# Kernel optimization log

Measured on AMD Instinct MI355X. Metric: run time of the kernel, lower is better.

The kernel has to match this reference:

```python
import jax, jax.numpy as jnp
import numpy as np

H, W = 4096, 4096
KH, KW = 16, 16


def setup_inputs() -> dict:
    key = jax.random.key(0)
    kx, kw = jax.random.split(key)
    x = jax.random.normal(kx, (H, W), dtype=jnp.float32)
    weight = jax.random.normal(kw, (KH, KW), dtype=jnp.float32)
    bias = jnp.zeros((1,), dtype=jnp.float32)
    return {"x": x, "weight": weight, "bias": bias}


def reference(x, weight, bias):
    # 2D valid cross-correlation (no kernel flip), single channel, + scalar bias.
    # lax.conv_general_dilated computes cross-correlation by default.
    lhs = x[None, None, :, :]          # [1,1,H,W]
    rhs = weight[None, None, :, :]     # [1,1,KH,KW]
    y = jax.lax.conv_general_dilated(
        lhs, rhs,
        window_strides=(1, 1),
        padding="VALID",
        dimension_numbers=("NCHW", "OIHW", "NCHW"),
    )[0, 0]                            # [H-KH+1, W-KW+1]
    return y + bias[0]
```

## Files before the change

### kernel.cpp

```cpp
#include <hip/hip_runtime.h>

#define IH 4096
#define IW 4096
#define KH 16
#define KW 16
#define OH 4081
#define OW 4081

#define TBR 64
#define TBC 256
#define LROWS 79
#define LCH 40
#define LSTR (LCH*8)

typedef short bf16x8 __attribute__((ext_vector_type(8)));
typedef float f32x16 __attribute__((ext_vector_type(16)));

static __device__ __forceinline__ unsigned int f2bf(float f) {
    unsigned int u = __float_as_uint(f);
    return (u + 0x7FFFu + ((u >> 16) & 1u)) >> 16;
}

__global__ void build_B(const float* __restrict__ wgt, unsigned short* __restrict__ Bt) {
    int idx = blockIdx.x * 256 + threadIdx.x;
    if (idx >= 16 * 32 * 48) return;
    int vp = idx % 48;
    int n  = (idx / 48) & 31;
    int u  = idx / (48 * 32);
    int t  = vp - n;
    float val = (t >= 0 && t < KW) ? wgt[u * KW + t] : 0.0f;
    Bt[idx] = (unsigned short)f2bf(val);
}

__global__ __launch_bounds__(256, 3)
void conv_mfma32(const float* __restrict__ x,
                 const unsigned short* __restrict__ Bt,
                 const float* __restrict__ bias,
                 float* __restrict__ out) {
    __shared__ unsigned short tile[LROWS * LSTR];

    const int tid  = threadIdx.x;
    const int lane = tid & 63;
    const int wv   = tid >> 6;
    const int rb   = wv >> 1;
    const int cb   = wv & 1;
    const int m    = lane & 31;
    const int hi   = lane >> 5;
    const int gy0  = blockIdx.y * TBR;
    const int gx0  = blockIdx.x * TBC;

    for (int idx = tid; idx < LROWS * 34; idx += 256) {
        int row = idx / 34;
        int c   = idx - row * 34;
        int gy  = gy0 + row;
        int gx  = gx0 + 8 * c;
        float4 q0 = make_float4(0.f, 0.f, 0.f, 0.f);
        float4 q1 = q0;
        if (gy < IH && gx < IW) {
            q0 = *reinterpret_cast<const float4*>(x + (size_t)gy * IW + gx);
            q1 = *reinterpret_cast<const float4*>(x + (size_t)gy * IW + gx + 4);
        }
        uint4 p;
        p.x = f2bf(q0.x) | (f2bf(q0.y) << 16);
        p.y = f2bf(q0.z) | (f2bf(q0.w) << 16);
        p.z = f2bf(q1.x) | (f2bf(q1.y) << 16);
        p.w = f2bf(q1.z) | (f2bf(q1.w) << 16);
        int s    = (row ^ (row >> 3)) & 7;
        int phys = c ^ s;
        *reinterpret_cast<uint4*>(&tile[row * LSTR + phys * 8]) = p;
    }
    __syncthreads();

    f32x16 acc0 = {0,0,0,0,0,0,0,0,0,0,0,0,0,0,0,0};
    f32x16 acc1 = {0,0,0,0,0,0,0,0,0,0,0,0,0,0,0,0};
    f32x16 acc2 = {0,0,0,0,0,0,0,0,0,0,0,0,0,0,0,0};
    f32x16 acc3 = {0,0,0,0,0,0,0,0,0,0,0,0,0,0,0,0};

    const int cB = cb * 16 + hi;
    const unsigned short* Blane = Bt + m * 48 + hi * 8;

    bf16x8 bc0 = *reinterpret_cast<const bf16x8*>(Blane + 0);
    bf16x8 bc1 = *reinterpret_cast<const bf16x8*>(Blane + 16);
    bf16x8 bc2 = *reinterpret_cast<const bf16x8*>(Blane + 32);

#pragma unroll
    for (int u = 0; u < KH; ++u) {
        bf16x8 bn0 = bc0, bn1 = bc1, bn2 = bc2;
        if (u + 1 < KH) {
            const unsigned short* Bu = Blane + (u + 1) * (32 * 48);
            bn0 = *reinterpret_cast<const bf16x8*>(Bu + 0);
            bn1 = *reinterpret_cast<const bf16x8*>(Bu + 16);
            bn2 = *reinterpret_cast<const bf16x8*>(Bu + 32);
        }

        const int rowA = rb * 32 + m + u;
        const int s    = (rowA ^ (rowA >> 3)) & 7;
        const unsigned short* rbase = &tile[rowA * LSTR];

        bf16x8 a[9];
#pragma unroll
        for (int d = 0; d < 9; ++d) {
            int phys = (cB + 2 * d) ^ s;
            a[d] = *reinterpret_cast<const bf16x8*>(rbase + phys * 8);
        }

        acc0 = __builtin_amdgcn_mfma_f32_32x32x16_bf16(a[0], bc0, acc0, 0, 0, 0);
        acc0 = __builtin_amdgcn_mfma_f32_32x32x16_bf16(a[1], bc1, acc0, 0, 0, 0);
        acc0 = __builtin_amdgcn_mfma_f32_32x32x16_bf16(a[2], bc2, acc0, 0, 0, 0);
        acc1 = __builtin_amdgcn_mfma_f32_32x32x16_bf16(a[2], bc0, acc1, 0, 0, 0);
        acc1 = __builtin_amdgcn_mfma_f32_32x32x16_bf16(a[3], bc1, acc1, 0, 0, 0);
        acc1 = __builtin_amdgcn_mfma_f32_32x32x16_bf16(a[4], bc2, acc1, 0, 0, 0);
        acc2 = __builtin_amdgcn_mfma_f32_32x32x16_bf16(a[4], bc0, acc2, 0, 0, 0);
        acc2 = __builtin_amdgcn_mfma_f32_32x32x16_bf16(a[5], bc1, acc2, 0, 0, 0);
        acc2 = __builtin_amdgcn_mfma_f32_32x32x16_bf16(a[6], bc2, acc2, 0, 0, 0);
        acc3 = __builtin_amdgcn_mfma_f32_32x32x16_bf16(a[6], bc0, acc3, 0, 0, 0);
        acc3 = __builtin_amdgcn_mfma_f32_32x32x16_bf16(a[7], bc1, acc3, 0, 0, 0);
        acc3 = __builtin_amdgcn_mfma_f32_32x32x16_bf16(a[8], bc2, acc3, 0, 0, 0);

        bc0 = bn0; bc1 = bn1; bc2 = bn2;
    }

    const float bv   = bias[0];
    const int   row0 = gy0 + rb * 32 + 4 * hi;
    const int   col0 = gx0 + cb * 128 + m;
    const bool  full = (gy0 + TBR <= OH) && (gx0 + TBC <= OW);

    const f32x16* accs[4] = {&acc0, &acc1, &acc2, &acc3};
#pragma unroll
    for (int g = 0; g < 4; ++g) {
        const f32x16 acc = *accs[g];
        const int col = col0 + g * 32;
        float* op = out + col;
        if (full) {
#pragma unroll
            for (int r = 0; r < 16; ++r) {
                int rr = row0 + (r & 3) + 8 * (r >> 2);
                op[(size_t)rr * OW] = acc[r] + bv;
            }
        } else if (col < OW) {
#pragma unroll
            for (int r = 0; r < 16; ++r) {
                int rr = row0 + (r & 3) + 8 * (r >> 2);
                if (rr < OH) op[(size_t)rr * OW] = acc[r] + bv;
            }
        }
    }
}

extern "C" void kernel_launch(void* const* d_in, const int* in_sizes, int n_in,
                              void* d_out, int out_size, void* d_ws, size_t ws_size,
                              hipStream_t stream) {
    const float* x  = (const float*)d_in[0];
    const float* w  = (const float*)d_in[1];
    const float* b  = (const float*)d_in[2];
    float* out = (float*)d_out;
    unsigned short* Bt = (unsigned short*)d_ws;

    build_B<<<96, 256, 0, stream>>>(w, Bt);

    dim3 grid((OW + TBC - 1) / TBC, (OH + TBR - 1) / TBR);
    conv_mfma32<<<grid, dim3(256), 0, stream>>>(x, Bt, b, out);
}
```

Measured before the change: 137.7 us.

## Halve column tile width, drop LDS swizzle, raise occupancy target

Shrinks the block tile from 256 to 128 output columns, so each wave keeps two MFMA accumulators instead of four and the shared tile shrinks. The launch bound is raised so more blocks can be resident per CU. The XOR swizzle on the LDS tile is replaced by a padded row stride of 168 elements, which is meant to avoid bank conflicts more cheaply. In exchange, the halo columns (extra input read and converted per block) make up a larger share of each tile, and there is less reuse of A fragments per wave.

```diff
diff --git a/kernel.cpp b/kernel.cpp
--- a/kernel.cpp
+++ b/kernel.cpp
@@ -8,10 +8,9 @@
 #define OW 4081
 
 #define TBR 64
-#define TBC 256
+#define TBC 128
 #define LROWS 79
-#define LCH 40
-#define LSTR (LCH*8)
+#define LSTR 168
 
 typedef short bf16x8 __attribute__((ext_vector_type(8)));
 typedef float f32x16 __attribute__((ext_vector_type(16)));
@@ -32,7 +31,7 @@
     Bt[idx] = (unsigned short)f2bf(val);
 }
 
-__global__ __launch_bounds__(256, 3)
+__global__ __launch_bounds__(256, 6)
 void conv_mfma32(const float* __restrict__ x,
                  const unsigned short* __restrict__ Bt,
                  const float* __restrict__ bias,
@@ -49,9 +48,9 @@
     const int gy0  = blockIdx.y * TBR;
     const int gx0  = blockIdx.x * TBC;
 
-    for (int idx = tid; idx < LROWS * 34; idx += 256) {
-        int row = idx / 34;
-        int c   = idx - row * 34;
+    for (int idx = tid; idx < LROWS * 18; idx += 256) {
+        int row = idx / 18;
+        int c   = idx - row * 18;
         int gy  = gy0 + row;
         int gx  = gx0 + 8 * c;
         float4 q0 = make_float4(0.f, 0.f, 0.f, 0.f);
@@ -65,18 +64,14 @@
         p.y = f2bf(q0.z) | (f2bf(q0.w) << 16);
         p.z = f2bf(q1.x) | (f2bf(q1.y) << 16);
         p.w = f2bf(q1.z) | (f2bf(q1.w) << 16);
-        int s    = (row ^ (row >> 3)) & 7;
-        int phys = c ^ s;
-        *reinterpret_cast<uint4*>(&tile[row * LSTR + phys * 8]) = p;
+        *reinterpret_cast<uint4*>(&tile[row * LSTR + c * 8]) = p;
     }
     __syncthreads();
 
     f32x16 acc0 = {0,0,0,0,0,0,0,0,0,0,0,0,0,0,0,0};
     f32x16 acc1 = {0,0,0,0,0,0,0,0,0,0,0,0,0,0,0,0};
-    f32x16 acc2 = {0,0,0,0,0,0,0,0,0,0,0,0,0,0,0,0};
-    f32x16 acc3 = {0,0,0,0,0,0,0,0,0,0,0,0,0,0,0,0};
 
-    const int cB = cb * 16 + hi;
+    const int cB = cb * 8 + hi;
     const unsigned short* Blane = Bt + m * 48 + hi * 8;
 
     bf16x8 bc0 = *reinterpret_cast<const bf16x8*>(Blane + 0);
@@ -94,41 +89,32 @@
         }
 
         const int rowA = rb * 32 + m + u;
-        const int s    = (rowA ^ (rowA >> 3)) & 7;
         const unsigned short* rbase = &tile[rowA * LSTR];
 
-        bf16x8 a[9];
-#pragma unroll
-        for (int d = 0; d < 9; ++d) {
-            int phys = (cB + 2 * d) ^ s;
-            a[d] = *reinterpret_cast<const bf16x8*>(rbase + phys * 8);
-        }
+        bf16x8 a0 = *reinterpret_cast<const bf16x8*>(rbase + (cB + 0) * 8);
+        bf16x8 a1 = *reinterpret_cast<const bf16x8*>(rbase + (cB + 2) * 8);
+        bf16x8 a2 = *reinterpret_cast<const bf16x8*>(rbase + (cB + 4) * 8);
+        bf16x8 a3 = *reinterpret_cast<const bf16x8*>(rbase + (cB + 6) * 8);
+        bf16x8 a4 = *reinterpret_cast<const bf16x8*>(rbase + (cB + 8) * 8);
 
-        acc0 = __builtin_amdgcn_mfma_f32_32x32x16_bf16(a[0], bc0, acc0, 0, 0, 0);
-        acc0 = __builtin_amdgcn_mfma_f32_32x32x16_bf16(a[1], bc1, acc0, 0, 0, 0);
-        acc0 = __builtin_amdgcn_mfma_f32_32x32x16_bf16(a[2], bc2, acc0, 0, 0, 0);
-        acc1 = __builtin_amdgcn_mfma_f32_32x32x16_bf16(a[2], bc0, acc1, 0, 0, 0);
-        acc1 = __builtin_amdgcn_mfma_f32_32x32x16_bf16(a[3], bc1, acc1, 0, 0, 0);
-        acc1 = __builtin_amdgcn_mfma_f32_32x32x16_bf16(a[4], bc2, acc1, 0, 0, 0);
-        acc2 = __builtin_amdgcn_mfma_f32_32x32x16_bf16(a[4], bc0, acc2, 0, 0, 0);
-        acc2 = __builtin_amdgcn_mfma_f32_32x32x16_bf16(a[5], bc1, acc2, 0, 0, 0);
-        acc2 = __builtin_amdgcn_mfma_f32_32x32x16_bf16(a[6], bc2, acc2, 0, 0, 0);
-        acc3 = __builtin_amdgcn_mfma_f32_32x32x16_bf16(a[6], bc0, acc3, 0, 0, 0);
-        acc3 = __builtin_amdgcn_mfma_f32_32x32x16_bf16(a[7], bc1, acc3, 0, 0, 0);
-        acc3 = __builtin_amdgcn_mfma_f32_32x32x16_bf16(a[8], bc2, acc3, 0, 0, 0);
+        acc0 = __builtin_amdgcn_mfma_f32_32x32x16_bf16(a0, bc0, acc0, 0, 0, 0);
+        acc0 = __builtin_amdgcn_mfma_f32_32x32x16_bf16(a1, bc1, acc0, 0, 0, 0);
+        acc0 = __builtin_amdgcn_mfma_f32_32x32x16_bf16(a2, bc2, acc0, 0, 0, 0);
+        acc1 = __builtin_amdgcn_mfma_f32_32x32x16_bf16(a2, bc0, acc1, 0, 0, 0);
+        acc1 = __builtin_amdgcn_mfma_f32_32x32x16_bf16(a3, bc1, acc1, 0, 0, 0);
+        acc1 = __builtin_amdgcn_mfma_f32_32x32x16_bf16(a4, bc2, acc1, 0, 0, 0);
 
         bc0 = bn0; bc1 = bn1; bc2 = bn2;
     }
 
     const float bv   = bias[0];
     const int   row0 = gy0 + rb * 32 + 4 * hi;
-    const int   col0 = gx0 + cb * 128 + m;
+    const int   col0 = gx0 + cb * 64 + m;
     const bool  full = (gy0 + TBR <= OH) && (gx0 + TBC <= OW);
 
-    const f32x16* accs[4] = {&acc0, &acc1, &acc2, &acc3};
 #pragma unroll
-    for (int g = 0; g < 4; ++g) {
-        const f32x16 acc = *accs[g];
+    for (int g = 0; g < 2; ++g) {
+        const f32x16 acc = g ? acc1 : acc0;
         const int col = col0 + g * 32;
         float* op = out + col;
         if (full) {
```

New measurement: 142.5 us. 3.5% more time.
